# Performance work log

Hardware: AMD Instinct MI355X
Metric: run time of the kernel (lower is better)

Reference implementation:

```python
import jax, jax.numpy as jnp
import numpy as np
from jax import lax

PADDING_L = 30  # causal: kernel_size - 1


def setup_inputs() -> dict:
    key = jax.random.key(0)
    k1, k2 = jax.random.split(key)
    T, B, C = 4096, 8, 1024
    H, K = 16, 31
    x = jax.random.normal(k1, (T, B, C), dtype=jnp.float32)
    weight = jax.random.normal(k2, (H, K), dtype=jnp.float32)
    return {"x": x, "weight": weight}


def reference(x, weight):
    # x: [T, B, C]; weight: [H, K]
    T, B, C = x.shape
    H, K = weight.shape
    R = C // H  # channels per head share the same kernel
    # weight_softmax=True: normalize kernel taps per head
    w = jax.nn.softmax(weight, axis=-1)            # [H, K]
    wc = jnp.repeat(w, R, axis=0)[:, None, :]      # [C, 1, K] depthwise kernel
    xb = jnp.transpose(x, (1, 2, 0))               # [B, C, T]
    # lightconv_cuda: out[b,c,t] = sum_k w[h(c),k] * x_pad[b,c,t+k],
    # left pad = padding_l, right pad = K-1-padding_l (cross-correlation)
    out = lax.conv_general_dilated(
        xb, wc,
        window_strides=(1,),
        padding=[(PADDING_L, K - 1 - PADDING_L)],
        feature_group_count=C,
        dimension_numbers=("NCH", "OIH", "NCH"),
    )                                              # [B, C, T]
    return jnp.transpose(out, (2, 0, 1))           # [T, B, C]
```

## Files before the change

### kernel.cpp

```cpp
#include <hip/hip_runtime.h>
#include <math.h>

#define T_DIM 4096
#define B_DIM 8
#define C_DIM 1024
#define H_DIM 16
#define K_DIM 31
#define PAD_L 30
#define TILE_T 32
#define WIN (TILE_T + K_DIM - 1)
#define BLOCK 256

typedef __attribute__((ext_vector_type(4))) float f32x4;

__device__ __forceinline__ void stage16(const float* g, float* l) {
    __builtin_amdgcn_global_load_lds(
        (const __attribute__((address_space(1))) void*)g,
        (__attribute__((address_space(3))) void*)l,
        16, 0, 0);
}

template <int J>
__device__ __forceinline__ void conv_step(const float* col,
                                          const float (&taps)[K_DIM],
                                          float (&acc)[TILE_T]) {
    const float xj = col[J * BLOCK];
    #pragma unroll
    for (int i = 0; i < TILE_T; ++i) {
        if (J - i >= 0 && J - i < K_DIM)
            acc[i] = fmaf(taps[J - i], xj, acc[i]);
    }
}

template <int J>
__device__ __forceinline__ void conv_all(const float* col,
                                         const float (&taps)[K_DIM],
                                         float (&acc)[TILE_T]) {
    if constexpr (J < WIN) {
        conv_step<J>(col, taps, acc);
        conv_all<J + 1>(col, taps, acc);
    }
}

__global__ __launch_bounds__(BLOCK, 2) void lightconv_kernel(
    const float* __restrict__ x,
    const float* __restrict__ w,
    float* __restrict__ out)
{
    __shared__ float tile[WIN][BLOCK];
    __shared__ float s_taps[4][K_DIM];

    const int tid    = threadIdx.x;
    const int lane   = tid & 63;
    const int wv     = tid >> 6;
    const int colBlk = blockIdx.x;
    const int tBlk   = blockIdx.y;
    const int t0     = tBlk * TILE_T;
    const long stride = (long)B_DIM * C_DIM;

    {
        const float* gbase = x + (long)(t0 - PAD_L) * stride
                               + colBlk * BLOCK + lane * 4;
        #pragma unroll
        for (int i = 0; i < 16; ++i) {
            const int r = wv * 16 + i;
            if (r < WIN) {
                if (t0 - PAD_L + r >= 0) {
                    stage16(gbase + (long)r * stride, &tile[r][0]);
                } else {
                    const f32x4 z = {0.0f, 0.0f, 0.0f, 0.0f};
                    *(f32x4*)&tile[r][lane * 4] = z;
                }
            }
        }
    }

    if (tid < 4) {
        const int c0 = (colBlk * BLOCK) % C_DIM;
        const int h  = (c0 >> 6) + tid;
        const float* wr = w + h * K_DIM;
        float m = -1e30f;
        #pragma unroll
        for (int k = 0; k < K_DIM; ++k) m = fmaxf(m, wr[k]);
        float s = 0.0f;
        #pragma unroll
        for (int k = 0; k < K_DIM; ++k) {
            float e = __expf(wr[k] - m);
            s_taps[tid][k] = e;
            s += e;
        }
        const float inv = 1.0f / s;
        #pragma unroll
        for (int k = 0; k < K_DIM; ++k) s_taps[tid][k] *= inv;
    }

    __syncthreads();

    float taps[K_DIM];
    #pragma unroll
    for (int k = 0; k < K_DIM; ++k) {
        taps[k] = __int_as_float(
            __builtin_amdgcn_readfirstlane(__float_as_int(s_taps[wv][k])));
    }

    float acc[TILE_T];
    #pragma unroll
    for (int i = 0; i < TILE_T; ++i) acc[i] = 0.0f;

    conv_all<0>(&tile[0][0] + tid, taps, acc);

    float* po = out + (long)t0 * stride + (colBlk * BLOCK + tid);
    #pragma unroll
    for (int i = 0; i < TILE_T; ++i)
        __builtin_nontemporal_store(acc[i], po + (long)i * stride);
}

extern "C" void kernel_launch(void* const* d_in, const int* in_sizes, int n_in,
                              void* d_out, int out_size, void* d_ws, size_t ws_size,
                              hipStream_t stream) {
    const float* x = (const float*)d_in[0];
    const float* w = (const float*)d_in[1];
    float* out = (float*)d_out;

    dim3 grid((B_DIM * C_DIM) / BLOCK, T_DIM / TILE_T);
    lightconv_kernel<<<grid, BLOCK, 0, stream>>>(x, w, out);
}
```

Measured before the change: 231.0 us.

## Stream time tiles through an LDS ring buffer with halo reuse and prefetch

Each block now processes eight consecutive 32-step time tiles. A 64-row LDS ring buffer keeps the 30-row halo from the previous tile, so halo rows are no longer reloaded. The next tile's rows are staged asynchronously while the second half of the convolution runs, and outputs are stored as soon as each is complete. Softmax of the taps is computed per wave in registers rather than through shared memory. The cost is fewer blocks (less parallelism in the grid) and two barriers per tile.

```diff
diff --git a/kernel.cpp b/kernel.cpp
--- a/kernel.cpp
+++ b/kernel.cpp
@@ -8,8 +8,10 @@
 #define K_DIM 31
 #define PAD_L 30
 #define TILE_T 32
-#define WIN (TILE_T + K_DIM - 1)
+#define WIN 62
 #define BLOCK 256
+#define RING_ROWS 64
+#define TPB 8
 
 typedef __attribute__((ext_vector_type(4))) float f32x4;
 
@@ -20,26 +22,68 @@
         16, 0, 0);
 }
 
-template <int J>
-__device__ __forceinline__ void conv_step(const float* col,
-                                          const float (&taps)[K_DIM],
-                                          float (&acc)[TILE_T]) {
-    const float xj = col[J * BLOCK];
-    #pragma unroll
-    for (int i = 0; i < TILE_T; ++i) {
-        if (J - i >= 0 && J - i < K_DIM)
-            acc[i] = fmaf(taps[J - i], xj, acc[i]);
+
+template <int TPAR, int J>
+__device__ __forceinline__ void conv_a(const float* col,
+                                       const float (&taps)[K_DIM],
+                                       float (&acc)[TILE_T]) {
+    if constexpr (J < 30) {
+        const float xj = col[((TPAR + J + 34) & 63) * BLOCK];
+        #pragma unroll
+        for (int i = 0; i <= J; ++i) {
+            if (i == J) acc[i] = taps[0] * xj;
+            else        acc[i] = fmaf(taps[J - i], xj, acc[i]);
+        }
+        conv_a<TPAR, J + 1>(col, taps, acc);
     }
 }
 
-template <int J>
-__device__ __forceinline__ void conv_all(const float* col,
-                                         const float (&taps)[K_DIM],
-                                         float (&acc)[TILE_T]) {
+template <int TPAR, int J>
+__device__ __forceinline__ void conv_b(const float* col,
+                                       const float (&taps)[K_DIM],
+                                       float (&acc)[TILE_T],
+                                       float* po, long stride) {
     if constexpr (J < WIN) {
-        conv_step<J>(col, taps, acc);
-        conv_all<J + 1>(col, taps, acc);
+        const float xj = col[((TPAR + J + 34) & 63) * BLOCK];
+        constexpr int ilo = J - 30;
+        constexpr int ihi = (J < TILE_T - 1) ? J : TILE_T - 1;
+        #pragma unroll
+        for (int i = ilo; i <= ihi; ++i) {
+            if (i == J) acc[i] = taps[0] * xj;
+            else        acc[i] = fmaf(taps[J - i], xj, acc[i]);
+        }
+        __builtin_nontemporal_store(acc[J - 30], po + (long)(J - 30) * stride);
+        conv_b<TPAR, J + 1>(col, taps, acc, po, stride);
     }
+}
+
+template <int TPAR>
+__device__ __forceinline__ void iter_body(
+    const float* __restrict__ x, float* __restrict__ out,
+    const float* col, float* lds0,
+    const float (&taps)[K_DIM],
+    long t0, int wv, int lane, int cc0, int tid, bool stage_next)
+{
+    const long stride = (long)B_DIM * C_DIM;
+    float acc[TILE_T];
+
+    conv_a<TPAR, 0>(col, taps, acc);
+
+    __syncthreads();
+
+    if (stage_next) {
+        const long g0 = t0 + TILE_T + wv * 8;
+        const float* gp = x + g0 * stride + cc0 + lane * 4;
+        float* lp = lds0 + ((TPAR + TILE_T + wv * 8) & 63) * BLOCK;
+        #pragma unroll
+        for (int i = 0; i < 8; ++i)
+            stage16(gp + (long)i * stride, lp + i * BLOCK);
+    }
+
+    float* po = out + t0 * stride + cc0 + tid;
+    conv_b<TPAR, 30>(col, taps, acc, po, stride);
+
+    __syncthreads();
 }
 
 __global__ __launch_bounds__(BLOCK, 2) void lightconv_kernel(
@@ -47,72 +91,63 @@
     const float* __restrict__ w,
     float* __restrict__ out)
 {
-    __shared__ float tile[WIN][BLOCK];
-    __shared__ float s_taps[4][K_DIM];
+    __shared__ float ring[RING_ROWS][BLOCK];
 
     const int tid    = threadIdx.x;
     const int lane   = tid & 63;
     const int wv     = tid >> 6;
     const int colBlk = blockIdx.x;
-    const int tBlk   = blockIdx.y;
-    const int t0     = tBlk * TILE_T;
+    const int tg     = blockIdx.y;
+    const int cc0    = colBlk * BLOCK;
     const long stride = (long)B_DIM * C_DIM;
+    const long tgbase = (long)tg * (TPB * TILE_T);
 
     {
-        const float* gbase = x + (long)(t0 - PAD_L) * stride
-                               + colBlk * BLOCK + lane * 4;
+        const int r0 = wv * 16;
+        const int rn = (wv == 3) ? 14 : 16;
         #pragma unroll
         for (int i = 0; i < 16; ++i) {
-            const int r = wv * 16 + i;
-            if (r < WIN) {
-                if (t0 - PAD_L + r >= 0) {
-                    stage16(gbase + (long)r * stride, &tile[r][0]);
+            if (i < rn) {
+                const long gr = tgbase - PAD_L + r0 + i;
+                const int slot = ((int)gr) & 63;
+                if (gr >= 0) {
+                    stage16(x + gr * stride + cc0 + lane * 4, &ring[slot][0]);
                 } else {
-                    const f32x4 z = {0.0f, 0.0f, 0.0f, 0.0f};
-                    *(f32x4*)&tile[r][lane * 4] = z;
+                    const f32x4 z = {0.f, 0.f, 0.f, 0.f};
+                    *(f32x4*)&ring[slot][lane * 4] = z;
                 }
             }
         }
     }
 
-    if (tid < 4) {
-        const int c0 = (colBlk * BLOCK) % C_DIM;
-        const int h  = (c0 >> 6) + tid;
-        const float* wr = w + h * K_DIM;
+    float taps[K_DIM];
+    {
+        const float* wr = w + (((colBlk & 3) << 2) + wv) * K_DIM;
+        float tv[K_DIM];
         float m = -1e30f;
         #pragma unroll
-        for (int k = 0; k < K_DIM; ++k) m = fmaxf(m, wr[k]);
-        float s = 0.0f;
+        for (int k = 0; k < K_DIM; ++k) { tv[k] = wr[k]; m = fmaxf(m, tv[k]); }
+        float s = 0.f;
         #pragma unroll
-        for (int k = 0; k < K_DIM; ++k) {
-            float e = __expf(wr[k] - m);
-            s_taps[tid][k] = e;
-            s += e;
-        }
+        for (int k = 0; k < K_DIM; ++k) { tv[k] = __expf(tv[k] - m); s += tv[k]; }
         const float inv = 1.0f / s;
         #pragma unroll
-        for (int k = 0; k < K_DIM; ++k) s_taps[tid][k] *= inv;
+        for (int k = 0; k < K_DIM; ++k)
+            taps[k] = __int_as_float(__builtin_amdgcn_readfirstlane(
+                          __float_as_int(tv[k] * inv)));
     }
 
     __syncthreads();
 
-    float taps[K_DIM];
-    #pragma unroll
-    for (int k = 0; k < K_DIM; ++k) {
-        taps[k] = __int_as_float(
-            __builtin_amdgcn_readfirstlane(__float_as_int(s_taps[wv][k])));
+    const float* col = &ring[0][0] + tid;
+    float* lds0 = &ring[0][0];
+    long t0 = tgbase;
+    #pragma unroll 1
+    for (int it = 0; it < TPB; ++it, t0 += TILE_T) {
+        const bool sn = (it < TPB - 1);
+        if (it & 1) iter_body<32>(x, out, col, lds0, taps, t0, wv, lane, cc0, tid, sn);
+        else        iter_body< 0>(x, out, col, lds0, taps, t0, wv, lane, cc0, tid, sn);
     }
-
-    float acc[TILE_T];
-    #pragma unroll
-    for (int i = 0; i < TILE_T; ++i) acc[i] = 0.0f;
-
-    conv_all<0>(&tile[0][0] + tid, taps, acc);
-
-    float* po = out + (long)t0 * stride + (colBlk * BLOCK + tid);
-    #pragma unroll
-    for (int i = 0; i < TILE_T; ++i)
-        __builtin_nontemporal_store(acc[i], po + (long)i * stride);
 }
 
 extern "C" void kernel_launch(void* const* d_in, const int* in_sizes, int n_in,
@@ -122,6 +157,6 @@
     const float* w = (const float*)d_in[1];
     float* out = (float*)d_out;
 
-    dim3 grid((B_DIM * C_DIM) / BLOCK, T_DIM / TILE_T);
+    dim3 grid((B_DIM * C_DIM) / BLOCK, T_DIM / (TPB * TILE_T));
     lightconv_kernel<<<grid, BLOCK, 0, stream>>>(x, w, out);
 }
```

Measured after the change: 237.4 us. +2.8%, slower.

## Halve time tile, stream stores inside conv loop, compute softmax taps per wave

Applied to the files above, without the earlier changes.

Shrinks the time tile from 32 to 16 rows, which makes the accumulator array smaller and lets launch bounds request three blocks per SM instead of two. Each output row is stored as soon as its accumulation finishes, and the first tap initialises the accumulator instead of zero-filling it. The tap softmax now runs in every wave with register values, removing the shared-memory tap buffer. The cost is a larger halo overhead per tile (46 staged rows for 16 outputs versus 61 for 32), so more redundant global reads, and every wave now does the softmax work.

```diff
diff --git a/kernel.cpp b/kernel.cpp
--- a/kernel.cpp
+++ b/kernel.cpp
@@ -7,9 +7,11 @@
 #define H_DIM 16
 #define K_DIM 31
 #define PAD_L 30
-#define TILE_T 32
-#define WIN (TILE_T + K_DIM - 1)
+#define HALO 30
+#define TILE_T 16
+#define WROWS (TILE_T + HALO)
 #define BLOCK 256
+#define CC 256
 
 typedef __attribute__((ext_vector_type(4))) float f32x4;
 
@@ -21,34 +23,32 @@
 }
 
 template <int J>
-__device__ __forceinline__ void conv_step(const float* col,
-                                          const float (&taps)[K_DIM],
-                                          float (&acc)[TILE_T]) {
-    const float xj = col[J * BLOCK];
-    #pragma unroll
-    for (int i = 0; i < TILE_T; ++i) {
-        if (J - i >= 0 && J - i < K_DIM)
-            acc[i] = fmaf(taps[J - i], xj, acc[i]);
+__device__ __forceinline__ void conv_all(const float* col,
+                                         const float (&taps)[K_DIM],
+                                         float (&acc)[TILE_T],
+                                         float* po, long stride) {
+    if constexpr (J < WROWS) {
+        const float xj = col[J * CC];
+        constexpr int ilo = (J > HALO) ? (J - HALO) : 0;
+        constexpr int ihi = (J < TILE_T - 1) ? J : TILE_T - 1;
+        #pragma unroll
+        for (int i = ilo; i <= ihi; ++i) {
+            if (i == J) acc[i] = taps[0] * xj;
+            else        acc[i] = fmaf(taps[J - i], xj, acc[i]);
+        }
+        if constexpr (J >= HALO)
+            __builtin_nontemporal_store(acc[J - HALO],
+                                        po + (long)(J - HALO) * stride);
+        conv_all<J + 1>(col, taps, acc, po, stride);
     }
 }
 
-template <int J>
-__device__ __forceinline__ void conv_all(const float* col,
-                                         const float (&taps)[K_DIM],
-                                         float (&acc)[TILE_T]) {
-    if constexpr (J < WIN) {
-        conv_step<J>(col, taps, acc);
-        conv_all<J + 1>(col, taps, acc);
-    }
-}
-
-__global__ __launch_bounds__(BLOCK, 2) void lightconv_kernel(
+__global__ __launch_bounds__(BLOCK, 3) void lightconv_kernel(
     const float* __restrict__ x,
     const float* __restrict__ w,
     float* __restrict__ out)
 {
-    __shared__ float tile[WIN][BLOCK];
-    __shared__ float s_taps[4][K_DIM];
+    __shared__ float tile[WROWS][CC];
 
     const int tid    = threadIdx.x;
     const int lane   = tid & 63;
@@ -56,63 +56,48 @@
     const int colBlk = blockIdx.x;
     const int tBlk   = blockIdx.y;
     const int t0     = tBlk * TILE_T;
+    const int cc0    = colBlk * CC;
     const long stride = (long)B_DIM * C_DIM;
 
     {
-        const float* gbase = x + (long)(t0 - PAD_L) * stride
-                               + colBlk * BLOCK + lane * 4;
+        const int r0 = wv * 12;
+        const int rn = (wv == 3) ? WROWS - 36 : 12;
+        const float* gbase = x + (long)(t0 - HALO) * stride + cc0 + lane * 4;
         #pragma unroll
-        for (int i = 0; i < 16; ++i) {
-            const int r = wv * 16 + i;
-            if (r < WIN) {
-                if (t0 - PAD_L + r >= 0) {
+        for (int i = 0; i < 12; ++i) {
+            if (i < rn) {
+                const int r = r0 + i;
+                if (t0 - HALO + r >= 0) {
                     stage16(gbase + (long)r * stride, &tile[r][0]);
                 } else {
-                    const f32x4 z = {0.0f, 0.0f, 0.0f, 0.0f};
-                    *(f32x4*)&tile[r][lane * 4] = z;
+                    *(f32x4*)&tile[r][lane * 4] = (f32x4){0.f, 0.f, 0.f, 0.f};
                 }
             }
         }
     }
 
-    if (tid < 4) {
-        const int c0 = (colBlk * BLOCK) % C_DIM;
-        const int h  = (c0 >> 6) + tid;
-        const float* wr = w + h * K_DIM;
+    float taps[K_DIM];
+    {
+        const float* wr = w + (((colBlk & 3) << 2) + wv) * K_DIM;
+        float tv[K_DIM];
         float m = -1e30f;
         #pragma unroll
-        for (int k = 0; k < K_DIM; ++k) m = fmaxf(m, wr[k]);
-        float s = 0.0f;
+        for (int k = 0; k < K_DIM; ++k) { tv[k] = wr[k]; m = fmaxf(m, tv[k]); }
+        float s = 0.f;
         #pragma unroll
-        for (int k = 0; k < K_DIM; ++k) {
-            float e = __expf(wr[k] - m);
-            s_taps[tid][k] = e;
-            s += e;
-        }
+        for (int k = 0; k < K_DIM; ++k) { tv[k] = __expf(tv[k] - m); s += tv[k]; }
         const float inv = 1.0f / s;
         #pragma unroll
-        for (int k = 0; k < K_DIM; ++k) s_taps[tid][k] *= inv;
+        for (int k = 0; k < K_DIM; ++k)
+            taps[k] = __int_as_float(__builtin_amdgcn_readfirstlane(
+                          __float_as_int(tv[k] * inv)));
     }
 
     __syncthreads();
 
-    float taps[K_DIM];
-    #pragma unroll
-    for (int k = 0; k < K_DIM; ++k) {
-        taps[k] = __int_as_float(
-            __builtin_amdgcn_readfirstlane(__float_as_int(s_taps[wv][k])));
-    }
-
     float acc[TILE_T];
-    #pragma unroll
-    for (int i = 0; i < TILE_T; ++i) acc[i] = 0.0f;
-
-    conv_all<0>(&tile[0][0] + tid, taps, acc);
-
-    float* po = out + (long)t0 * stride + (colBlk * BLOCK + tid);
-    #pragma unroll
-    for (int i = 0; i < TILE_T; ++i)
-        __builtin_nontemporal_store(acc[i], po + (long)i * stride);
+    float* po = out + (long)t0 * stride + cc0 + tid;
+    conv_all<0>(&tile[0][0] + tid, taps, acc, po, stride);
 }
 
 extern "C" void kernel_launch(void* const* d_in, const int* in_sizes, int n_in,
@@ -122,6 +107,6 @@
     const float* w = (const float*)d_in[1];
     float* out = (float*)d_out;
 
-    dim3 grid((B_DIM * C_DIM) / BLOCK, T_DIM / TILE_T);
+    dim3 grid((B_DIM * C_DIM) / CC, T_DIM / TILE_T);
     lightconv_kernel<<<grid, BLOCK, 0, stream>>>(x, w, out);
 }
```

After: 231.4 us. About the same (+0.2%).
